# Optimization experiments

Hardware: AMD Instinct MI355X
Metric: run time of the kernel (lower is better)

## Reference

```python
import jax, jax.numpy as jnp
import numpy as np

B, S, DM, H = 2, 2048, 1024, 16
D = DM // H  # head dim = 64


def setup_inputs() -> dict:
    key = jax.random.key(0)
    k1, k2, k3, k4, k5 = jax.random.split(key, 5)
    hidden_states = jax.random.normal(k1, (B, S, DM), dtype=jnp.float32)
    attention_mask = jnp.zeros((B, 1, S, S), dtype=jnp.float32)
    position_ids = jnp.broadcast_to(jnp.arange(S, dtype=jnp.int32), (B, S))
    # nn.Linear weights stored as (out, in); x @ W.T
    Wq = jax.random.normal(k2, (DM, DM), dtype=jnp.float32) * 0.02
    Wk = jax.random.normal(k3, (DM, DM), dtype=jnp.float32) * 0.02
    Wv = jax.random.normal(k4, (DM, DM), dtype=jnp.float32) * 0.02
    return {"hidden_states": hidden_states, "attention_mask": attention_mask,
            "position_ids": position_ids, "Wq": Wq, "Wk": Wk, "Wv": Wv}


def _rotate_half(x):
    h = x.shape[-1] // 2
    return jnp.concatenate((-x[..., h:], x[..., :h]), axis=-1)


def _rope_cos_sin(position_ids, dtype):
    # inv_freq: (D/2,)
    inv_freq = 1.0 / (10000.0 ** (jnp.arange(0, D, 2, dtype=jnp.float32) / D))
    # freqs: (B, S, D/2)
    freqs = position_ids.astype(jnp.float32)[:, :, None] * inv_freq[None, None, :]
    emb = jnp.concatenate((freqs, freqs), axis=-1)  # (B, S, D)
    return jnp.cos(emb).astype(dtype), jnp.sin(emb).astype(dtype)


def reference(hidden_states, attention_mask, position_ids, Wq, Wk, Wv):
    def split_heads(x):  # (B,S,DM) -> (B,H,S,D)
        return x.reshape(B, S, H, D).transpose(0, 2, 1, 3)

    q = split_heads(hidden_states @ Wq.T)
    k = split_heads(hidden_states @ Wk.T)
    v = split_heads(hidden_states @ Wv.T)

    q = q * (D ** -0.5)

    cos, sin = _rope_cos_sin(position_ids, q.dtype)
    cos = cos[:, None, :, :]  # unsqueeze head dim -> (B,1,S,D)
    sin = sin[:, None, :, :]
    q = q * cos + _rotate_half(q) * sin
    k = k * cos + _rotate_half(k) * sin

    # (B,H,S,S)
    scores = jnp.einsum('bhqd,bhkd->bhqk', q, k) + attention_mask
    probs = jax.nn.softmax(scores.astype(jnp.float32), axis=-1).astype(q.dtype)
    ctx = jnp.einsum('bhqk,bhkd->bhqd', probs, v)  # (B,H,S,D)
    ctx = ctx.transpose(0, 2, 1, 3).reshape(B, S, DM)
    return ctx
```

## Files before the change

### kernel.cpp

```cpp
#include <hip/hip_runtime.h>
#include <math.h>

#define B  2
#define S  2048
#define DM 1024
#define H  16
#define Dh 64
#define BH (B*H)

typedef short  bf16x8 __attribute__((ext_vector_type(8)));
typedef float  f32x4  __attribute__((ext_vector_type(4)));

__device__ __forceinline__ unsigned short f2bf(float f) {
    unsigned u = __float_as_uint(f);
    u = (u + 0x7fffu + ((u >> 16) & 1u)) >> 16;
    return (unsigned short)u;
}

__device__ __forceinline__ unsigned cvt_pk_bf16(float lo, float hi) {
    unsigned r;
    asm("v_cvt_pk_bf16_f32 %0, %1, %2" : "=v"(r) : "v"(lo), "v"(hi));
    return r;
}

__device__ __forceinline__ void lds_barrier() {
    asm volatile("s_waitcnt lgkmcnt(0)" ::: "memory");
    __builtin_amdgcn_s_barrier();
    asm volatile("" ::: "memory");
}

__global__ __launch_bounds__(256) void cast_kernel(const float* __restrict__ X,
                                                   const float* __restrict__ Wq,
                                                   const float* __restrict__ Wk,
                                                   const float* __restrict__ Wv,
                                                   unsigned short* __restrict__ Xb,
                                                   unsigned short* __restrict__ Wb) {
    const long c = (long)(blockIdx.x * 256 + threadIdx.x) * 4;
    const float* src;
    unsigned short* dst;
    if (c < 4194304L) {
        src = X + c;  dst = Xb + c;
    } else {
        const long c2 = c - 4194304L;
        const int  wi = (int)(c2 >> 20);
        const long r  = c2 & 1048575L;
        src = (wi == 0 ? Wq : (wi == 1 ? Wk : Wv)) + r;
        dst = Wb + c2;
    }
    const float4 v = *(const float4*)src;
    ushort4 o;
    o.x = f2bf(v.x); o.y = f2bf(v.y); o.z = f2bf(v.z); o.w = f2bf(v.w);
    *(ushort4*)dst = o;
}

__global__ __launch_bounds__(256) void rope_tab_kernel(const int* __restrict__ pos,
                                                       float* __restrict__ Tab) {
    const int idx = blockIdx.x * 256 + threadIdx.x;
    const int i  = idx & 31;
    const int bs = idx >> 5;
    const float p   = (float)pos[bs];
    const float inv = exp2f(-(float)i * 0.41524101186092029f);
    float sn, cs;
    sincosf(p * inv, &sn, &cs);
    ((float2*)Tab)[idx] = make_float2(cs, sn);
}

__device__ __forceinline__ void gload_lds16(const unsigned short* g, unsigned short* l) {
    __builtin_amdgcn_global_load_lds(
        (const __attribute__((address_space(1))) unsigned int*)g,
        (__attribute__((address_space(3))) unsigned int*)l,
        16, 0, 0);
}

__global__ __launch_bounds__(256) void qkv_gemm(const unsigned short* __restrict__ Xb,
                                                const unsigned short* __restrict__ Wb,
                                                const float* __restrict__ Tab,
                                                unsigned short* __restrict__ Qb,
                                                unsigned short* __restrict__ Kb,
                                                unsigned short* __restrict__ Vb) {
    __shared__ __align__(16) unsigned short As[128 * 32];
    __shared__ __align__(16) unsigned short Bs[128 * 32];
    __shared__ __align__(16) unsigned short Es[64 * 136];

    const int tid  = threadIdx.x;
    const int w    = tid >> 6;
    const int lane = tid & 63;
    const int col  = lane & 15;
    const int quad = lane >> 4;
    const int m0 = blockIdx.x * 128;
    const int n0 = blockIdx.y * 128;
    const int mw = (w & 1) * 64;
    const int nw = (w >> 1) * 64;

    const int srow = lane >> 2;
    const int sk8  = (((lane & 3) ^ (srow & 3))) * 8;

    f32x4 acc[4][4] = {};

    for (int k0 = 0; k0 < 1024; k0 += 32) {
        __syncthreads();
        #pragma unroll
        for (int it = 0; it < 2; ++it) {
            const int rbase = w * 16 + it * 64;
            gload_lds16(Xb + (size_t)(m0 + rbase + srow) * 1024 + k0 + sk8,
                        &As[rbase * 32]);
            gload_lds16(Wb + (size_t)(n0 + rbase + srow) * 1024 + k0 + sk8,
                        &Bs[rbase * 32]);
        }
        __syncthreads();

        const int fs = (quad ^ (col & 3)) * 8;
        bf16x8 a[4], bb[4];
        #pragma unroll
        for (int i = 0; i < 4; ++i)
            a[i] = *(const bf16x8*)&As[(mw + i * 16 + col) * 32 + fs];
        #pragma unroll
        for (int j = 0; j < 4; ++j)
            bb[j] = *(const bf16x8*)&Bs[(nw + j * 16 + col) * 32 + fs];
        #pragma unroll
        for (int i = 0; i < 4; ++i)
            #pragma unroll
            for (int j = 0; j < 4; ++j)
                acc[i][j] = __builtin_amdgcn_mfma_f32_16x16x32_bf16(a[i], bb[j], acc[i][j], 0, 0, 0);
    }

    const int wsel = n0 >> 10;
    const int hh0  = (n0 & 1023) >> 6;
    const int bb2  = m0 >> 11;
    const int ssb  = m0 & 2047;

    if (wsel == 2) {
        #pragma unroll
        for (int half = 0; half < 2; ++half) {
            __syncthreads();
            if ((w >> 1) == half) {
                #pragma unroll
                for (int i = 0; i < 4; ++i) {
                    const int sl = mw + i * 16 + quad * 4;
                    #pragma unroll
                    for (int j = 0; j < 4; ++j) {
                        const int dl = j * 16 + col;
                        ushort4 ov;
                        ov.x = f2bf(acc[i][j][0]); ov.y = f2bf(acc[i][j][1]);
                        ov.z = f2bf(acc[i][j][2]); ov.w = f2bf(acc[i][j][3]);
                        *(ushort4*)&Es[dl * 136 + sl] = ov;
                    }
                }
            }
            __syncthreads();
            #pragma unroll
            for (int k = 0; k < 4; ++k) {
                const int c  = tid + k * 256;
                const int dl = c >> 4;
                const int s8 = (c & 15) * 8;
                const int d  = half * 64 + dl;
                const bf16x8 v = *(const bf16x8*)&Es[dl * 136 + s8];
                *(bf16x8*)(Vb + ((size_t)(bb2 * H + hh0 + (d >> 6)) * Dh + (d & 63)) * S
                           + ssb + s8) = v;
            }
        }
    } else {
        unsigned short* dp = (wsel == 0) ? Qb : Kb;
        const float qscale = (wsel == 0) ? 0.125f : 1.0f;
        #pragma unroll
        for (int half = 0; half < 2; ++half) {
            __syncthreads();
            if ((w & 1) == half) {
                #pragma unroll
                for (int i = 0; i < 4; ++i) {
                    #pragma unroll
                    for (int r = 0; r < 4; ++r) {
                        const int rl = i * 16 + quad * 4 + r;
                        const int ss = ssb + half * 64 + rl;
                        const float2 t0 = ((const float2*)Tab)[(size_t)(bb2 * S + ss) * 32 + col];
                        const float2 t1 = ((const float2*)Tab)[(size_t)(bb2 * S + ss) * 32 + col + 16];
                        const float a0 = acc[i][0][r] * qscale, a1 = acc[i][1][r] * qscale;
                        const float a2 = acc[i][2][r] * qscale, a3 = acc[i][3][r] * qscale;
                        unsigned short* e = &Es[rl * 136 + nw];
                        e[col]      = f2bf(a0 * t0.x - a2 * t0.y);
                        e[col + 16] = f2bf(a1 * t1.x - a3 * t1.y);
                        e[col + 32] = f2bf(a2 * t0.x + a0 * t0.y);
                        e[col + 48] = f2bf(a3 * t1.x + a1 * t1.y);
                    }
                }
            }
            __syncthreads();
            #pragma unroll
            for (int k = 0; k < 4; ++k) {
                const int c  = tid + k * 256;
                const int rl = c >> 4;
                const int d8 = (c & 15) * 8;
                const bf16x8 v = *(const bf16x8*)&Es[rl * 136 + d8];
                *(bf16x8*)(dp + ((size_t)(bb2 * H + hh0 + (d8 >> 6)) * S
                                 + ssb + half * 64 + rl) * Dh + (d8 & 63)) = v;
            }
        }
    }
}

#define KSd 72
#define LOG2E  1.4426950408889634f
#define NEG8L (-11.541560327111707f)
#define NT (S / 64)

__global__ __launch_bounds__(256) void attn_kernel(const unsigned short* __restrict__ Q,
                                                   const unsigned short* __restrict__ K,
                                                   const unsigned short* __restrict__ V,
                                                   const float* __restrict__ mask,
                                                   float* __restrict__ out) {
    __shared__ __align__(16) unsigned short Ks[2][64 * KSd];
    __shared__ __align__(16) unsigned short Vt[2][64 * KSd];
    __shared__ __align__(16) unsigned short Ps[4 * 32 * KSd];

    const int tid  = threadIdx.x;
    const int w    = tid >> 6;
    const int lane = tid & 63;
    const int col  = lane & 15;
    const int quad = lane >> 4;
    const int bh   = blockIdx.y;
    const int b    = bh >> 4, h = bh & 15;
    const int q0   = blockIdx.x * 128;
    const int qw   = q0 + w * 32;

    const int srow = tid >> 3;
    const int sc8  = (tid & 7) * 8;

    bf16x8 qa[2][2];
    #pragma unroll
    for (int u = 0; u < 2; ++u) {
        const unsigned short* qrow = Q + ((size_t)bh * S + qw + u * 16 + col) * Dh;
        qa[u][0] = *(const bf16x8*)(qrow + quad * 8);
        qa[u][1] = *(const bf16x8*)(qrow + 32 + quad * 8);
    }

    f32x4 o[4][2] = {};
    float lsum[2] = {0.f, 0.f};
    const float* mbase = mask + (size_t)b * S * S;
    unsigned short* pw = Ps + w * 32 * KSd;
    const unsigned short* Kbase = K + (size_t)bh * S * Dh;
    const unsigned short* Vbase = V + (size_t)bh * Dh * S;

    bf16x8 kp[2], vp[2];
    float4 mv[4][2];
    #pragma unroll
    for (int cc = 0; cc < 2; ++cc) {
        kp[cc] = *(const bf16x8*)(Kbase + (size_t)(srow + cc * 32) * Dh + sc8);
        vp[cc] = *(const bf16x8*)(Vbase + (size_t)(srow + cc * 32) * S + sc8);
    }
    #pragma unroll
    for (int u = 0; u < 2; ++u)
        #pragma unroll
        for (int f = 0; f < 4; ++f)
            mv[f][u] = *(const float4*)(mbase + (size_t)(qw + u * 16 + col) * S
                                        + f * 16 + quad * 4);
    #pragma unroll
    for (int cc = 0; cc < 2; ++cc) {
        const int row = srow + cc * 32;
        *(bf16x8*)&Ks[0][row * KSd + sc8] = kp[cc];
        *(bf16x8*)&Vt[0][row * KSd + sc8] = vp[cc];
    }
    #pragma unroll
    for (int cc = 0; cc < 2; ++cc) {
        kp[cc] = *(const bf16x8*)(Kbase + (size_t)(64 + srow + cc * 32) * Dh + sc8);
        vp[cc] = *(const bf16x8*)(Vbase + (size_t)(srow + cc * 32) * S + 64 + sc8);
    }
    lds_barrier();

    for (int kt = 0; kt < NT; ++kt) {
        const int cur = kt & 1;

        f32x4 sc[4][2] = {};
        #pragma unroll
        for (int f = 0; f < 4; ++f) {
            const bf16x8 ka0 = *(const bf16x8*)&Ks[cur][(f * 16 + col) * KSd + quad * 8];
            const bf16x8 ka1 = *(const bf16x8*)&Ks[cur][(f * 16 + col) * KSd + 32 + quad * 8];
            #pragma unroll
            for (int u = 0; u < 2; ++u) {
                sc[f][u] = __builtin_amdgcn_mfma_f32_16x16x32_bf16(ka0, qa[u][0], sc[f][u], 0, 0, 0);
                sc[f][u] = __builtin_amdgcn_mfma_f32_16x16x32_bf16(ka1, qa[u][1], sc[f][u], 0, 0, 0);
            }
        }

        #pragma unroll
        for (int u = 0; u < 2; ++u) {
            #pragma unroll
            for (int f = 0; f < 4; ++f) {
                sc[f][u][0] += mv[f][u].x; sc[f][u][1] += mv[f][u].y;
                sc[f][u][2] += mv[f][u].z; sc[f][u][3] += mv[f][u].w;
            }
            #pragma unroll
            for (int f = 0; f < 4; ++f)
                #pragma unroll
                for (int r = 0; r < 4; ++r) {
                    const float pv = __builtin_amdgcn_exp2f(
                        __builtin_fmaf(sc[f][u][r], LOG2E, NEG8L));
                    sc[f][u][r] = pv;
                    lsum[u] += pv;
                }
            unsigned short* pq = pw + (u * 16 + col) * KSd;
            #pragma unroll
            for (int f = 0; f < 4; ++f) {
                *(uint2*)&pq[f * 16 + quad * 4] =
                    make_uint2(cvt_pk_bf16(sc[f][u][0], sc[f][u][1]),
                               cvt_pk_bf16(sc[f][u][2], sc[f][u][3]));
            }
        }

        if (kt + 1 < NT) {
            #pragma unroll
            for (int u = 0; u < 2; ++u)
                #pragma unroll
                for (int f = 0; f < 4; ++f)
                    mv[f][u] = *(const float4*)(mbase + (size_t)(qw + u * 16 + col) * S
                                                + (kt + 1) * 64 + f * 16 + quad * 4);
        }

        if (kt + 1 < NT) {
            const int nxt = cur ^ 1;
            #pragma unroll
            for (int cc = 0; cc < 2; ++cc) {
                const int row = srow + cc * 32;
                *(bf16x8*)&Ks[nxt][row * KSd + sc8] = kp[cc];
                *(bf16x8*)&Vt[nxt][row * KSd + sc8] = vp[cc];
            }
            if (kt + 2 < NT) {
                #pragma unroll
                for (int cc = 0; cc < 2; ++cc) {
                    kp[cc] = *(const bf16x8*)(Kbase + (size_t)((kt + 2) * 64 + srow + cc * 32) * Dh + sc8);
                    vp[cc] = *(const bf16x8*)(Vbase + (size_t)(srow + cc * 32) * S + (kt + 2) * 64 + sc8);
                }
            }
        }

        asm volatile("s_waitcnt lgkmcnt(0)" ::: "memory");
        __builtin_amdgcn_sched_barrier(0);

        #pragma unroll
        for (int kc = 0; kc < 2; ++kc) {
            bf16x8 pb[2];
            #pragma unroll
            for (int u = 0; u < 2; ++u)
                pb[u] = *(const bf16x8*)&pw[(u * 16 + col) * KSd + kc * 32 + quad * 8];
            #pragma unroll
            for (int g = 0; g < 4; ++g) {
                const bf16x8 va = *(const bf16x8*)&Vt[cur][(g * 16 + col) * KSd + kc * 32 + quad * 8];
                #pragma unroll
                for (int u = 0; u < 2; ++u)
                    o[g][u] = __builtin_amdgcn_mfma_f32_16x16x32_bf16(va, pb[u], o[g][u], 0, 0, 0);
            }
        }
        lds_barrier();
    }

    #pragma unroll
    for (int u = 0; u < 2; ++u) {
        lsum[u] += __shfl_xor(lsum[u], 16, 64);
        lsum[u] += __shfl_xor(lsum[u], 32, 64);
    }

    #pragma unroll
    for (int u = 0; u < 2; ++u) {
        const float inv = 1.f / lsum[u];
        float* op = out + ((size_t)b * S + qw + u * 16 + col) * DM + h * Dh + quad * 4;
        #pragma unroll
        for (int g = 0; g < 4; ++g) {
            float4 ov;
            ov.x = o[g][u][0] * inv; ov.y = o[g][u][1] * inv;
            ov.z = o[g][u][2] * inv; ov.w = o[g][u][3] * inv;
            *(float4*)(op + g * 16) = ov;
        }
    }
}

extern "C" void kernel_launch(void* const* d_in, const int* in_sizes, int n_in,
                              void* d_out, int out_size, void* d_ws, size_t ws_size,
                              hipStream_t stream) {
    const float* hs   = (const float*)d_in[0];
    const float* mask = (const float*)d_in[1];
    const int*   pos  = (const int*)  d_in[2];
    const float* Wq   = (const float*)d_in[3];
    const float* Wk   = (const float*)d_in[4];
    const float* Wv   = (const float*)d_in[5];
    float* out = (float*)d_out;

    unsigned short* Xb = (unsigned short*)d_ws;
    unsigned short* Wb = Xb + 4194304;
    unsigned short* Qb = Wb + 3145728;
    unsigned short* Kb = Qb + 4194304;
    unsigned short* Vb = Kb + 4194304;
    float*          Tab = (float*)(Vb + 4194304);

    cast_kernel<<<7168, 256, 0, stream>>>(hs, Wq, Wk, Wv, Xb, Wb);
    rope_tab_kernel<<<512, 256, 0, stream>>>(pos, Tab);
    qkv_gemm<<<dim3(32, 24), 256, 0, stream>>>(Xb, Wb, Tab, Qb, Kb, Vb);
    attn_kernel<<<dim3(S / 128, BH), 256, 0, stream>>>(Qb, Kb, Vb, mask, out);
}
```

Baseline: 219.9 us.

## Enlarge attention blocks to 512 threads and remap GEMM tile order

The attention kernel now runs 8 waves per block covering 256 queries, so each K/V tile staged in shared memory is reused by twice as many query rows. Each thread now loads a single K and V vector per tile instead of two. Separately, the QKV GEMM remaps block indices so consecutive workgroups land on different chiplets/XCDs with grouped tiles, aiming for better L2 locality. The change halves the number of attention blocks, which may reduce occupancy and increases shared memory per block.

```diff
diff --git a/kernel.cpp b/kernel.cpp
--- a/kernel.cpp
+++ b/kernel.cpp
@@ -87,8 +87,10 @@
     const int lane = tid & 63;
     const int col  = lane & 15;
     const int quad = lane >> 4;
-    const int m0 = blockIdx.x * 128;
-    const int n0 = blockIdx.y * 128;
+    const int orig = blockIdx.y * 32 + blockIdx.x;
+    const int wg   = (orig & 7) * 96 + (orig >> 3);
+    const int m0 = (wg / 24) * 128;
+    const int n0 = (wg % 24) * 128;
     const int mw = (w & 1) * 64;
     const int nw = (w >> 1) * 64;
 
@@ -203,14 +205,14 @@
 #define NEG8L (-11.541560327111707f)
 #define NT (S / 64)
 
-__global__ __launch_bounds__(256) void attn_kernel(const unsigned short* __restrict__ Q,
+__global__ __launch_bounds__(512) void attn_kernel(const unsigned short* __restrict__ Q,
                                                    const unsigned short* __restrict__ K,
                                                    const unsigned short* __restrict__ V,
                                                    const float* __restrict__ mask,
                                                    float* __restrict__ out) {
     __shared__ __align__(16) unsigned short Ks[2][64 * KSd];
     __shared__ __align__(16) unsigned short Vt[2][64 * KSd];
-    __shared__ __align__(16) unsigned short Ps[4 * 32 * KSd];
+    __shared__ __align__(16) unsigned short Ps[8 * 32 * KSd];
 
     const int tid  = threadIdx.x;
     const int w    = tid >> 6;
@@ -219,7 +221,7 @@
     const int quad = lane >> 4;
     const int bh   = blockIdx.y;
     const int b    = bh >> 4, h = bh & 15;
-    const int q0   = blockIdx.x * 128;
+    const int q0   = blockIdx.x * 256;
     const int qw   = q0 + w * 32;
 
     const int srow = tid >> 3;
@@ -240,30 +242,20 @@
     const unsigned short* Kbase = K + (size_t)bh * S * Dh;
     const unsigned short* Vbase = V + (size_t)bh * Dh * S;
 
-    bf16x8 kp[2], vp[2];
+    bf16x8 kp, vp;
     float4 mv[4][2];
-    #pragma unroll
-    for (int cc = 0; cc < 2; ++cc) {
-        kp[cc] = *(const bf16x8*)(Kbase + (size_t)(srow + cc * 32) * Dh + sc8);
-        vp[cc] = *(const bf16x8*)(Vbase + (size_t)(srow + cc * 32) * S + sc8);
-    }
+    kp = *(const bf16x8*)(Kbase + (size_t)srow * Dh + sc8);
+    vp = *(const bf16x8*)(Vbase + (size_t)srow * S + sc8);
     #pragma unroll
     for (int u = 0; u < 2; ++u)
         #pragma unroll
         for (int f = 0; f < 4; ++f)
             mv[f][u] = *(const float4*)(mbase + (size_t)(qw + u * 16 + col) * S
                                         + f * 16 + quad * 4);
-    #pragma unroll
-    for (int cc = 0; cc < 2; ++cc) {
-        const int row = srow + cc * 32;
-        *(bf16x8*)&Ks[0][row * KSd + sc8] = kp[cc];
-        *(bf16x8*)&Vt[0][row * KSd + sc8] = vp[cc];
-    }
-    #pragma unroll
-    for (int cc = 0; cc < 2; ++cc) {
-        kp[cc] = *(const bf16x8*)(Kbase + (size_t)(64 + srow + cc * 32) * Dh + sc8);
-        vp[cc] = *(const bf16x8*)(Vbase + (size_t)(srow + cc * 32) * S + 64 + sc8);
-    }
+    *(bf16x8*)&Ks[0][srow * KSd + sc8] = kp;
+    *(bf16x8*)&Vt[0][srow * KSd + sc8] = vp;
+    kp = *(const bf16x8*)(Kbase + (size_t)(64 + srow) * Dh + sc8);
+    vp = *(const bf16x8*)(Vbase + (size_t)srow * S + 64 + sc8);
     lds_barrier();
 
     for (int kt = 0; kt < NT; ++kt) {
@@ -317,18 +309,11 @@
 
         if (kt + 1 < NT) {
             const int nxt = cur ^ 1;
-            #pragma unroll
-            for (int cc = 0; cc < 2; ++cc) {
-                const int row = srow + cc * 32;
-                *(bf16x8*)&Ks[nxt][row * KSd + sc8] = kp[cc];
-                *(bf16x8*)&Vt[nxt][row * KSd + sc8] = vp[cc];
-            }
+            *(bf16x8*)&Ks[nxt][srow * KSd + sc8] = kp;
+            *(bf16x8*)&Vt[nxt][srow * KSd + sc8] = vp;
             if (kt + 2 < NT) {
-                #pragma unroll
-                for (int cc = 0; cc < 2; ++cc) {
-                    kp[cc] = *(const bf16x8*)(Kbase + (size_t)((kt + 2) * 64 + srow + cc * 32) * Dh + sc8);
-                    vp[cc] = *(const bf16x8*)(Vbase + (size_t)(srow + cc * 32) * S + (kt + 2) * 64 + sc8);
-                }
+                kp = *(const bf16x8*)(Kbase + (size_t)((kt + 2) * 64 + srow) * Dh + sc8);
+                vp = *(const bf16x8*)(Vbase + (size_t)srow * S + (kt + 2) * 64 + sc8);
             }
         }
 
@@ -393,5 +378,5 @@
     cast_kernel<<<7168, 256, 0, stream>>>(hs, Wq, Wk, Wv, Xb, Wb);
     rope_tab_kernel<<<512, 256, 0, stream>>>(pos, Tab);
     qkv_gemm<<<dim3(32, 24), 256, 0, stream>>>(Xb, Wb, Tab, Qb, Kb, Vb);
-    attn_kernel<<<dim3(S / 128, BH), 256, 0, stream>>>(Qb, Kb, Vb, mask, out);
-}
+    attn_kernel<<<dim3(S / 256, BH), 512, 0, stream>>>(Qb, Kb, Vb, mask, out);
+}
```

Measured after the change: 231.4 us. +5.3%, slower.

## Double-buffer QKV GEMM with 256x256 tiles and 512-thread blocks

Applied to the files above, without the earlier changes.

Rewrites the QKV projection GEMM to use 256x256 output tiles, 512 threads and a 64-wide K step. Global-to-LDS loads are double-buffered with explicit vmcnt waits so the next tile loads while the current one is multiplied. The XOR-swizzled LDS layout is widened to 8 chunks, and the RoPE/transpose epilogue is restructured into four passes over a shared staging buffer. The larger tiles cut global traffic per FLOP, but the grid drops to 192 blocks, fewer than the number of CUs, and each block needs much more LDS.

```diff
diff --git a/kernel.cpp b/kernel.cpp
--- a/kernel.cpp
+++ b/kernel.cpp
@@ -72,58 +72,82 @@
         16, 0, 0);
 }
 
-__global__ __launch_bounds__(256) void qkv_gemm(const unsigned short* __restrict__ Xb,
-                                                const unsigned short* __restrict__ Wb,
-                                                const float* __restrict__ Tab,
-                                                unsigned short* __restrict__ Qb,
-                                                unsigned short* __restrict__ Kb,
-                                                unsigned short* __restrict__ Vb) {
-    __shared__ __align__(16) unsigned short As[128 * 32];
-    __shared__ __align__(16) unsigned short Bs[128 * 32];
-    __shared__ __align__(16) unsigned short Es[64 * 136];
+__global__ __launch_bounds__(512, 2) void qkv_gemm(const unsigned short* __restrict__ Xb,
+                                                   const unsigned short* __restrict__ Wb,
+                                                   const float* __restrict__ Tab,
+                                                   unsigned short* __restrict__ Qb,
+                                                   unsigned short* __restrict__ Kb,
+                                                   unsigned short* __restrict__ Vb) {
+    __shared__ __align__(16) unsigned short As[2][256 * 64];
+    __shared__ __align__(16) unsigned short Bs[2][256 * 64];
 
     const int tid  = threadIdx.x;
     const int w    = tid >> 6;
     const int lane = tid & 63;
     const int col  = lane & 15;
     const int quad = lane >> 4;
-    const int m0 = blockIdx.x * 128;
-    const int n0 = blockIdx.y * 128;
-    const int mw = (w & 1) * 64;
-    const int nw = (w >> 1) * 64;
-
-    const int srow = lane >> 2;
-    const int sk8  = (((lane & 3) ^ (srow & 3))) * 8;
-
-    f32x4 acc[4][4] = {};
-
-    for (int k0 = 0; k0 < 1024; k0 += 32) {
-        __syncthreads();
-        #pragma unroll
-        for (int it = 0; it < 2; ++it) {
-            const int rbase = w * 16 + it * 64;
-            gload_lds16(Xb + (size_t)(m0 + rbase + srow) * 1024 + k0 + sk8,
-                        &As[rbase * 32]);
-            gload_lds16(Wb + (size_t)(n0 + rbase + srow) * 1024 + k0 + sk8,
-                        &Bs[rbase * 32]);
-        }
-        __syncthreads();
-
-        const int fs = (quad ^ (col & 3)) * 8;
-        bf16x8 a[4], bb[4];
-        #pragma unroll
-        for (int i = 0; i < 4; ++i)
-            a[i] = *(const bf16x8*)&As[(mw + i * 16 + col) * 32 + fs];
-        #pragma unroll
-        for (int j = 0; j < 4; ++j)
-            bb[j] = *(const bf16x8*)&Bs[(nw + j * 16 + col) * 32 + fs];
-        #pragma unroll
-        for (int i = 0; i < 4; ++i)
-            #pragma unroll
-            for (int j = 0; j < 4; ++j)
-                acc[i][j] = __builtin_amdgcn_mfma_f32_16x16x32_bf16(a[i], bb[j], acc[i][j], 0, 0, 0);
-    }
-
+    const int wr   = w >> 2;
+    const int wn   = w & 3;
+    const int m0 = blockIdx.x * 256;
+    const int n0 = blockIdx.y * 256;
+
+    f32x4 acc[8][4] = {};
+
+#define QKV_STAGE(BUF, T) do {                                                 \
+    const int kk_ = (T) * 64;                                                  \
+    unsigned short* Ab_ = &As[BUF][(w * 64) * 8];                              \
+    unsigned short* Bb_ = &Bs[BUF][(w * 64) * 8];                              \
+    _Pragma("unroll")                                                          \
+    for (int a_ = 0; a_ < 4; ++a_) {                                           \
+        const int cid_ = a_ * 512 + tid;                                       \
+        const int row_ = cid_ >> 3;                                            \
+        const int gof_ = ((cid_ & 7) ^ (row_ & 7)) << 3;                       \
+        gload_lds16(Xb + (size_t)(m0 + row_) * 1024 + kk_ + gof_,              \
+                    Ab_ + a_ * 4096);                                          \
+        gload_lds16(Wb + (size_t)(n0 + row_) * 1024 + kk_ + gof_,              \
+                    Bb_ + a_ * 4096);                                          \
+    }                                                                          \
+} while (0)
+
+    QKV_STAGE(0, 0);
+    QKV_STAGE(1, 1);
+
+    for (int t = 0; t < 16; ++t) {
+        const int cb = t & 1;
+        if (t < 15) asm volatile("s_waitcnt vmcnt(8)" ::: "memory");
+        else        asm volatile("s_waitcnt vmcnt(0)" ::: "memory");
+        lds_barrier();
+
+        const unsigned short* Ac = &As[cb][0];
+        const unsigned short* Bc = &Bs[cb][0];
+        #pragma unroll
+        for (int kc = 0; kc < 2; ++kc) {
+            bf16x8 af[8], bfr[4];
+            #pragma unroll
+            for (int i = 0; i < 8; ++i) {
+                const int row = wr * 128 + i * 16 + col;
+                const int sl  = ((kc * 4 + quad) ^ (row & 7)) * 8;
+                af[i] = *(const bf16x8*)&Ac[row * 64 + sl];
+            }
+            #pragma unroll
+            for (int j = 0; j < 4; ++j) {
+                const int row = wn * 64 + j * 16 + col;
+                const int sl  = ((kc * 4 + quad) ^ (row & 7)) * 8;
+                bfr[j] = *(const bf16x8*)&Bc[row * 64 + sl];
+            }
+            #pragma unroll
+            for (int i = 0; i < 8; ++i)
+                #pragma unroll
+                for (int j = 0; j < 4; ++j)
+                    acc[i][j] = __builtin_amdgcn_mfma_f32_16x16x32_bf16(af[i], bfr[j], acc[i][j], 0, 0, 0);
+        }
+
+        lds_barrier();
+        if (t + 2 < 16) QKV_STAGE(cb, t + 2);
+    }
+#undef QKV_STAGE
+
+    unsigned short* Es = (unsigned short*)&As[0][0];
     const int wsel = n0 >> 10;
     const int hh0  = (n0 & 1023) >> 6;
     const int bb2  = m0 >> 11;
@@ -131,52 +155,52 @@
 
     if (wsel == 2) {
         #pragma unroll
-        for (int half = 0; half < 2; ++half) {
-            __syncthreads();
-            if ((w >> 1) == half) {
-                #pragma unroll
-                for (int i = 0; i < 4; ++i) {
-                    const int sl = mw + i * 16 + quad * 4;
+        for (int s = 0; s < 4; ++s) {
+            if (wn == s) {
+                #pragma unroll
+                for (int i = 0; i < 8; ++i) {
+                    const int sl = wr * 128 + i * 16 + quad * 4;
                     #pragma unroll
                     for (int j = 0; j < 4; ++j) {
                         const int dl = j * 16 + col;
                         ushort4 ov;
                         ov.x = f2bf(acc[i][j][0]); ov.y = f2bf(acc[i][j][1]);
                         ov.z = f2bf(acc[i][j][2]); ov.w = f2bf(acc[i][j][3]);
-                        *(ushort4*)&Es[dl * 136 + sl] = ov;
+                        *(ushort4*)&Es[dl * 264 + sl] = ov;
                     }
                 }
             }
-            __syncthreads();
+            lds_barrier();
             #pragma unroll
             for (int k = 0; k < 4; ++k) {
-                const int c  = tid + k * 256;
-                const int dl = c >> 4;
-                const int s8 = (c & 15) * 8;
-                const int d  = half * 64 + dl;
-                const bf16x8 v = *(const bf16x8*)&Es[dl * 136 + s8];
-                *(bf16x8*)(Vb + ((size_t)(bb2 * H + hh0 + (d >> 6)) * Dh + (d & 63)) * S
-                           + ssb + s8) = v;
-            }
+                const int c  = tid + k * 512;
+                const int dl = c >> 5;
+                const int s8 = (c & 31) * 8;
+                *(bf16x8*)(Vb + ((size_t)(bb2 * H + hh0 + s) * Dh + dl) * S + ssb + s8)
+                    = *(const bf16x8*)&Es[dl * 264 + s8];
+            }
+            lds_barrier();
         }
     } else {
         unsigned short* dp = (wsel == 0) ? Qb : Kb;
         const float qscale = (wsel == 0) ? 0.125f : 1.0f;
         #pragma unroll
-        for (int half = 0; half < 2; ++half) {
-            __syncthreads();
-            if ((w & 1) == half) {
-                #pragma unroll
-                for (int i = 0; i < 4; ++i) {
+        for (int s = 0; s < 4; ++s) {
+            if (wr == (s >> 1)) {
+                const int io = (s & 1) * 4;
+                #pragma unroll
+                for (int i2 = 0; i2 < 4; ++i2) {
                     #pragma unroll
                     for (int r = 0; r < 4; ++r) {
-                        const int rl = i * 16 + quad * 4 + r;
-                        const int ss = ssb + half * 64 + rl;
+                        const int rl = i2 * 16 + quad * 4 + r;
+                        const int ss = ssb + s * 64 + rl;
                         const float2 t0 = ((const float2*)Tab)[(size_t)(bb2 * S + ss) * 32 + col];
                         const float2 t1 = ((const float2*)Tab)[(size_t)(bb2 * S + ss) * 32 + col + 16];
-                        const float a0 = acc[i][0][r] * qscale, a1 = acc[i][1][r] * qscale;
-                        const float a2 = acc[i][2][r] * qscale, a3 = acc[i][3][r] * qscale;
-                        unsigned short* e = &Es[rl * 136 + nw];
+                        const float a0 = acc[io + i2][0][r] * qscale;
+                        const float a1 = acc[io + i2][1][r] * qscale;
+                        const float a2 = acc[io + i2][2][r] * qscale;
+                        const float a3 = acc[io + i2][3][r] * qscale;
+                        unsigned short* e = &Es[rl * 264 + wn * 64];
                         e[col]      = f2bf(a0 * t0.x - a2 * t0.y);
                         e[col + 16] = f2bf(a1 * t1.x - a3 * t1.y);
                         e[col + 32] = f2bf(a2 * t0.x + a0 * t0.y);
@@ -184,16 +208,17 @@
                     }
                 }
             }
-            __syncthreads();
+            lds_barrier();
             #pragma unroll
             for (int k = 0; k < 4; ++k) {
-                const int c  = tid + k * 256;
-                const int rl = c >> 4;
-                const int d8 = (c & 15) * 8;
-                const bf16x8 v = *(const bf16x8*)&Es[rl * 136 + d8];
-                *(bf16x8*)(dp + ((size_t)(bb2 * H + hh0 + (d8 >> 6)) * S
-                                 + ssb + half * 64 + rl) * Dh + (d8 & 63)) = v;
-            }
+                const int c  = tid + k * 512;
+                const int rl = c >> 5;
+                const int c8 = (c & 31) * 8;
+                *(bf16x8*)(dp + ((size_t)(bb2 * H + hh0 + (c8 >> 6)) * S
+                                 + ssb + s * 64 + rl) * Dh + (c8 & 63))
+                    = *(const bf16x8*)&Es[rl * 264 + c8];
+            }
+            lds_barrier();
         }
     }
 }
@@ -392,6 +417,6 @@
 
     cast_kernel<<<7168, 256, 0, stream>>>(hs, Wq, Wk, Wv, Xb, Wb);
     rope_tab_kernel<<<512, 256, 0, stream>>>(pos, Tab);
-    qkv_gemm<<<dim3(32, 24), 256, 0, stream>>>(Xb, Wb, Tab, Qb, Kb, Vb);
+    qkv_gemm<<<dim3(16, 12), 512, 0, stream>>>(Xb, Wb, Tab, Qb, Kb, Vb);
     attn_kernel<<<dim3(S / 128, BH), 256, 0, stream>>>(Qb, Kb, Vb, mask, out);
 }
```

After: 228.1 us. 1.04x slower.
